# Kernel optimization log

Measured on AMD Instinct MI355X. Metric: run time of the kernel, lower is better.

The kernel has to match this reference:

```python
import jax, jax.numpy as jnp
import numpy as np

WINDOW_SIZE = 11
SIGMA = 1.5
CHANNELS = 3
PAD = WINDOW_SIZE // 2


def make_window():
    xs = np.arange(WINDOW_SIZE)
    g = np.exp(-((xs - WINDOW_SIZE // 2) ** 2) / (2.0 * SIGMA ** 2))
    g = g / g.sum()
    w2d = np.outer(g, g).astype(np.float32)  # [11,11]
    # depthwise kernel in OIHW with groups=3: [3,1,11,11]
    return jnp.asarray(np.broadcast_to(w2d, (CHANNELS, 1, WINDOW_SIZE, WINDOW_SIZE)).copy())


def setup_inputs() -> dict:
    key = jax.random.key(0)
    k1, k2 = jax.random.split(key)
    x = jax.random.uniform(k1, (16, 3, 512, 512), dtype=jnp.float32)
    y = jax.random.uniform(k2, (16, 3, 512, 512), dtype=jnp.float32)
    window = make_window()
    return {"x": x, "y": y, "window": window}


def _dwconv(img, window):
    # depthwise 2D conv, padding=5, groups=3 (NCHW / OIHW)
    return jax.lax.conv_general_dilated(
        img, window,
        window_strides=(1, 1),
        padding=[(PAD, PAD), (PAD, PAD)],
        feature_group_count=CHANNELS,
        dimension_numbers=("NCHW", "OIHW", "NCHW"),
    )


def reference(x, y, window):
    mu1 = _dwconv(x, window)
    mu2 = _dwconv(y, window)
    mu1_sq = mu1 * mu1
    mu2_sq = mu2 * mu2
    mu1_mu2 = mu1 * mu2
    sigma1_sq = _dwconv(x * x, window) - mu1_sq
    sigma2_sq = _dwconv(y * y, window) - mu2_sq
    sigma12 = _dwconv(x * y, window) - mu1_mu2
    c1 = 0.01 ** 2
    c2 = 0.03 ** 2
    ssim = ((2.0 * mu1_mu2 + c1) * (2.0 * sigma12 + c2)) / (
        (mu1_sq + mu2_sq + c1) * (sigma1_sq + sigma2_sq + c2))
    return jnp.mean(ssim)
```

## Files before the change

### kernel.cpp

```cpp
#include <hip/hip_runtime.h>


#define IMG_H 512
#define IMG_W 512
#define NC    48

constexpr int TW = 64;
constexpr int TH = 16;
constexpr int VW = 76;
constexpr int NBLK = (IMG_W / TW) * (IMG_H / TH) * NC;

__global__ __launch_bounds__(256, 6)
void ssim_fused(const float* __restrict__ x, const float* __restrict__ y,
                const float* __restrict__ w, double* __restrict__ part,
                int use_atomic)
{
    __shared__ __align__(16) float vv[5][TH][VW];
    __shared__ float wsum[4];

    const int tid = threadIdx.x;
    const int x0 = blockIdx.x * TW - 8;
    const int y0 = blockIdx.y * TH - 5;
    const float* __restrict__ xp = x + (size_t)blockIdx.z * (IMG_H * IMG_W);
    const float* __restrict__ yp = y + (size_t)blockIdx.z * (IMG_H * IMG_W);

    float g[11];
    {
        const float g5inv = 1.0f / sqrtf(w[55 + 5]);
        #pragma unroll
        for (int k = 0; k < 11; ++k)
            g[k] = __uint_as_float(
                (unsigned)__builtin_amdgcn_readfirstlane(
                    (int)__float_as_uint(w[55 + k] * g5inv)));
    }

    const bool interior = (y0 >= 0) & (y0 + 25 < IMG_H)
                        & (x0 + 2 >= 0) & (x0 + 76 < IMG_W);

    for (int t = tid; t < 75 * 4; t += 256) {
        const int c   = t % 75;
        const int r0  = (t / 75) << 2;
        const int gc  = x0 + c + 2;
        const int gr0 = y0 + r0;
        float xv[14], yv[14], xxv[14], yyv[14], xyv[14];
        if (interior) {
            const unsigned base = (unsigned)(gr0 * IMG_W + gc);
            #pragma unroll
            for (int k = 0; k < 14; ++k) {
                const float a = xp[base + (unsigned)(k * IMG_W)];
                const float b = yp[base + (unsigned)(k * IMG_W)];
                xv[k] = a; yv[k] = b;
                xxv[k] = a * a; yyv[k] = b * b; xyv[k] = a * b;
            }
        } else {
            const int  cc  = min(max(gc, 0), IMG_W - 1);
            const bool okc = ((unsigned)gc < (unsigned)IMG_W);
            #pragma unroll
            for (int k = 0; k < 14; ++k) {
                const int  gr = gr0 + k;
                const int  cr = min(max(gr, 0), IMG_H - 1);
                const bool ok = okc & ((unsigned)gr < (unsigned)IMG_H);
                const unsigned idx = (unsigned)(cr * IMG_W + cc);
                const float a = ok ? xp[idx] : 0.0f;
                const float b = ok ? yp[idx] : 0.0f;
                xv[k] = a; yv[k] = b;
                xxv[k] = a * a; yyv[k] = b * b; xyv[k] = a * b;
            }
        }
        #pragma unroll
        for (int j = 0; j < 4; ++j) {
            float s0 = 0.f, s1 = 0.f, s2 = 0.f, s3 = 0.f, s4 = 0.f;
            #pragma unroll
            for (int k = 0; k < 11; ++k) {
                const float gk = g[k];
                s0 = fmaf(gk, xv[j + k],  s0);
                s1 = fmaf(gk, yv[j + k],  s1);
                s2 = fmaf(gk, xxv[j + k], s2);
                s3 = fmaf(gk, yyv[j + k], s3);
                s4 = fmaf(gk, xyv[j + k], s4);
            }
            vv[0][r0 + j][c] = s0;
            vv[1][r0 + j][c] = s1;
            vv[2][r0 + j][c] = s2;
            vv[3][r0 + j][c] = s3;
            vv[4][r0 + j][c] = s4;
        }
    }
    __syncthreads();

    const int r  = tid >> 4;
    const int j0 = (tid & 15) << 2;

    float acc[5][4];
    #pragma unroll
    for (int q = 0; q < 5; ++q) {
        const float4* vp = (const float4*)(&vv[q][r][j0]);
        const float4 A = vp[0], B = vp[1], C = vp[2], D = vp[3];
        const float win[16] = {A.x, A.y, A.z, A.w, B.x, B.y, B.z, B.w,
                               C.x, C.y, C.z, C.w, D.x, D.y, D.z, D.w};
        #pragma unroll
        for (int t = 0; t < 4; ++t) {
            float s = 0.f;
            #pragma unroll
            for (int k = 0; k < 11; ++k) s = fmaf(g[k], win[t + 1 + k], s);
            acc[q][t] = s;
        }
    }

    const float C1 = 1e-4f;
    const float C2 = 9e-4f;
    float local = 0.0f;
    #pragma unroll
    for (int t = 0; t < 4; ++t) {
        const float m1 = acc[0][t], m2 = acc[1][t];
        const float m1s = m1 * m1, m2s = m2 * m2, m12 = m1 * m2;
        const float v1  = acc[2][t] - m1s;
        const float v2  = acc[3][t] - m2s;
        const float v12 = acc[4][t] - m12;
        const float num = (2.0f * m12 + C1) * (2.0f * v12 + C2);
        const float den = (m1s + m2s + C1) * (v1 + v2 + C2);
        local += num / den;
    }

    #pragma unroll
    for (int off = 32; off > 0; off >>= 1)
        local += __shfl_down(local, off, 64);
    if ((tid & 63) == 0) wsum[tid >> 6] = local;
    __syncthreads();
    if (tid == 0) {
        const double blk = (double)wsum[0] + (double)wsum[1]
                         + (double)wsum[2] + (double)wsum[3];
        if (use_atomic) {
            atomicAdd(part, blk);
        } else {
            const int bflat = blockIdx.x
                            + gridDim.x * (blockIdx.y + gridDim.y * blockIdx.z);
            part[bflat] = blk;
        }
    }
}

__global__ void ssim_reduce(const double* __restrict__ part, float* __restrict__ out,
                            int n)
{
    __shared__ double s[256];
    double t = 0.0;
    for (int i = threadIdx.x; i < n; i += 256) t += part[i];
    s[threadIdx.x] = t;
    __syncthreads();
    for (int off = 128; off > 0; off >>= 1) {
        if (threadIdx.x < off) s[threadIdx.x] += s[threadIdx.x + off];
        __syncthreads();
    }
    if (threadIdx.x == 0)
        out[0] = (float)(s[0] / (double)((size_t)NC * IMG_H * IMG_W));
}

extern "C" void kernel_launch(void* const* d_in, const int* in_sizes, int n_in,
                              void* d_out, int out_size, void* d_ws, size_t ws_size,
                              hipStream_t stream)
{
    const float* x = (const float*)d_in[0];
    const float* y = (const float*)d_in[1];
    const float* w = (const float*)d_in[2];
    double* part = (double*)d_ws;

    const bool fits = ws_size >= (size_t)NBLK * sizeof(double);
    dim3 grid(IMG_W / TW, IMG_H / TH, NC);

    if (fits) {
        ssim_fused<<<grid, 256, 0, stream>>>(x, y, w, part, 0);
        ssim_reduce<<<1, 256, 0, stream>>>(part, (float*)d_out, NBLK);
    } else {
        hipMemsetAsync(d_ws, 0, sizeof(double), stream);
        ssim_fused<<<grid, 256, 0, stream>>>(x, y, w, part, 1);
        ssim_reduce<<<1, 256, 0, stream>>>(part, (float*)d_out, 1);
    }
}
```

Before: 184.2 us.

## Store vertical partial sums as fp16 and use packed fdot2 for horizontal pass

The vertical-pass results are now stored in shared memory as half precision, halving LDS footprint. The horizontal 11-tap filter uses packed fp16 dot products (fdot2) with fp16 weights renormalized by their sum. Launch bounds raise the occupancy target and the division becomes a hardware reciprocal. This trades accuracy (fp16 rounding of sigma terms computed as differences) for fewer LDS bytes and ALU ops, with some risk to numerical tolerance.

```diff
diff --git a/kernel.cpp b/kernel.cpp
--- a/kernel.cpp
+++ b/kernel.cpp
@@ -1,4 +1,5 @@
 #include <hip/hip_runtime.h>
+#include <hip/hip_fp16.h>
 
 
 #define IMG_H 512
@@ -7,15 +8,20 @@
 
 constexpr int TW = 64;
 constexpr int TH = 16;
-constexpr int VW = 76;
 constexpr int NBLK = (IMG_W / TW) * (IMG_H / TH) * NC;
 
-__global__ __launch_bounds__(256, 6)
+typedef _Float16 v2h __attribute__((ext_vector_type(2)));
+
+static __device__ __forceinline__ v2h as_h2(unsigned u) {
+    union { unsigned u; v2h h; } x; x.u = u; return x.h;
+}
+
+__global__ __launch_bounds__(256, 8)
 void ssim_fused(const float* __restrict__ x, const float* __restrict__ y,
                 const float* __restrict__ w, double* __restrict__ part,
                 int use_atomic)
 {
-    __shared__ __align__(16) float vv[5][TH][VW];
+    __shared__ __align__(16) __half vvH[5][TH][80];
     __shared__ float wsum[4];
 
     const int tid = threadIdx.x;
@@ -33,6 +39,16 @@
                 (unsigned)__builtin_amdgcn_readfirstlane(
                     (int)__float_as_uint(w[55 + k] * g5inv)));
     }
+    v2h g2[6];
+    float hsum = 0.0f;
+    #pragma unroll
+    for (int p = 0; p < 6; ++p) {
+        const float lo = g[2 * p];
+        const float hi = (p < 5) ? g[2 * p + 1] : 0.0f;
+        g2[p] = v2h{(_Float16)lo, (_Float16)hi};
+        hsum += (float)g2[p].x + (float)g2[p].y;
+    }
+    const float hnorm = 1.0f / hsum;
 
     const bool interior = (y0 >= 0) & (y0 + 25 < IMG_H)
                         & (x0 + 2 >= 0) & (x0 + 76 < IMG_W);
@@ -79,32 +95,43 @@
                 s3 = fmaf(gk, yyv[j + k], s3);
                 s4 = fmaf(gk, xyv[j + k], s4);
             }
-            vv[0][r0 + j][c] = s0;
-            vv[1][r0 + j][c] = s1;
-            vv[2][r0 + j][c] = s2;
-            vv[3][r0 + j][c] = s3;
-            vv[4][r0 + j][c] = s4;
-        }
-    }
+            vvH[0][r0 + j][c] = __float2half(s0);
+            vvH[1][r0 + j][c] = __float2half(s1);
+            vvH[2][r0 + j][c] = __float2half(s2);
+            vvH[3][r0 + j][c] = __float2half(s3);
+            vvH[4][r0 + j][c] = __float2half(s4);
+        }
+    }
+    if (tid < 80) vvH[tid >> 4][tid & 15][75] = __half(0.0f);
     __syncthreads();
 
     const int r  = tid >> 4;
-    const int j0 = (tid & 15) << 2;
+    const int i  = tid & 15;
+    const int w0  = (i >> 1) << 2;
+    const int dlt = (i & 1) << 1;
 
     float acc[5][4];
     #pragma unroll
     for (int q = 0; q < 5; ++q) {
-        const float4* vp = (const float4*)(&vv[q][r][j0]);
-        const float4 A = vp[0], B = vp[1], C = vp[2], D = vp[3];
-        const float win[16] = {A.x, A.y, A.z, A.w, B.x, B.y, B.z, B.w,
-                               C.x, C.y, C.z, C.w, D.x, D.y, D.z, D.w};
-        #pragma unroll
-        for (int t = 0; t < 4; ++t) {
-            float s = 0.f;
-            #pragma unroll
-            for (int k = 0; k < 11; ++k) s = fmaf(g[k], win[t + 1 + k], s);
-            acc[q][t] = s;
-        }
+        const unsigned* rowp = (const unsigned*)&vvH[q][r][0];
+        unsigned A[12];
+        *(uint4*)&A[0] = *(const uint4*)(rowp + w0);
+        *(uint4*)&A[4] = *(const uint4*)(rowp + w0 + 4);
+        *(uint4*)&A[8] = *(const uint4*)(rowp + w0 + 8);
+        unsigned S[7];
+        #pragma unroll
+        for (int m = 0; m < 7; ++m)
+            S[m] = (A[dlt + m] >> 16) | (A[dlt + m + 1] << 16);
+        float a0 = 0.f, a1 = 0.f, a2 = 0.f, a3 = 0.f;
+        #pragma unroll
+        for (int p = 0; p < 6; ++p) {
+            a0 = __builtin_amdgcn_fdot2(as_h2(S[p]),           g2[p], a0, false);
+            a1 = __builtin_amdgcn_fdot2(as_h2(A[dlt + 1 + p]), g2[p], a1, false);
+            a2 = __builtin_amdgcn_fdot2(as_h2(S[1 + p]),       g2[p], a2, false);
+            a3 = __builtin_amdgcn_fdot2(as_h2(A[dlt + 2 + p]), g2[p], a3, false);
+        }
+        acc[q][0] = a0 * hnorm; acc[q][1] = a1 * hnorm;
+        acc[q][2] = a2 * hnorm; acc[q][3] = a3 * hnorm;
     }
 
     const float C1 = 1e-4f;
@@ -119,7 +146,7 @@
         const float v12 = acc[4][t] - m12;
         const float num = (2.0f * m12 + C1) * (2.0f * v12 + C2);
         const float den = (m1s + m2s + C1) * (v1 + v2 + C2);
-        local += num / den;
+        local += num * __builtin_amdgcn_rcpf(den);
     }
 
     #pragma unroll
```

After: 369.8 us. +100.8%, slower.
